# Kernel tuning notes

Hardware: AMD Instinct MI355X
Metric: run time of the kernel (lower is better)

The kernel has to match this reference:

```python
import jax, jax.numpy as jnp
import numpy as np

B, N, D = 4, 2048, 1024
H, HD = 16, 64
MAX_SEQ = 4096
INNER = H * HD


def setup_inputs() -> dict:
    key = jax.random.key(0)
    ks = jax.random.split(key, 5)
    s = 0.02
    return {
        "x": jax.random.normal(ks[0], (B, N, D), dtype=jnp.float32),
        "ln_gamma": jnp.ones((D,), jnp.float32),
        "ln_beta": jnp.zeros((D,), jnp.float32),
        "w_qkv": jax.random.normal(ks[1], (D, 3 * INNER), dtype=jnp.float32) * s,
        "w_out": jax.random.normal(ks[2], (INNER, D), dtype=jnp.float32) * s,
        "b_out": jnp.zeros((D,), jnp.float32),
    }


def _rope_tables(n, head_dim):
    inv_freq = 1.0 / (10000.0 ** (jnp.arange(0, head_dim, 2, dtype=jnp.float32) / head_dim))
    pos = jnp.arange(n, dtype=jnp.float32)
    ang = pos[:, None] * inv_freq[None, :]  # [n, hd/2]
    return jnp.sin(ang), jnp.cos(ang)


def reference(x, ln_gamma, ln_beta, w_qkv, w_out, b_out):
    b, n, d = x.shape
    # LayerNorm
    mu = jnp.mean(x, axis=-1, keepdims=True)
    var = jnp.var(x, axis=-1, keepdims=True)
    xn = (x - mu) / jnp.sqrt(var + 1e-5) * ln_gamma + ln_beta
    # QKV projection (no bias)
    qkv = xn @ w_qkv  # [b, n, 3*inner]
    q, k, v = jnp.split(qkv, 3, axis=-1)
    def to_heads(t):
        return t.reshape(b, n, H, HD).transpose(0, 2, 1, 3)  # b h n d
    q, k, v = to_heads(q), to_heads(k), to_heads(v)
    # RoPE (half-split rotation, as in source)
    sin, cos = _rope_tables(n, HD)  # [n, hd/2]
    sin = sin[None, None]
    cos = cos[None, None]
    half = HD // 2
    def rotate(t):
        t1, t2 = t[..., :half], t[..., half:]
        return jnp.concatenate([t1 * cos - t2 * sin, t2 * cos + t1 * sin], axis=-1)
    qr, kr = rotate(q), rotate(k)
    scale = HD ** -0.5
    scores = jnp.einsum('bhid,bhjd->bhij', qr, kr) * scale
    probs = jax.nn.softmax(scores, axis=-1)
    out = jnp.einsum('bhij,bhjd->bhid', probs, v)
    out = out.transpose(0, 2, 1, 3).reshape(b, n, INNER)
    return out @ w_out + b_out
```

## Files before the change

kernel.cpp:

```cpp
#include <hip/hip_runtime.h>
#include <hip/hip_bf16.h>

#define Bb   4
#define Nn   2048
#define Dd   1024
#define Hh   16
#define HDd  64
#define IN3  3072
#define RR   8192

typedef __attribute__((ext_vector_type(8))) short short8;
typedef __attribute__((ext_vector_type(4))) float floatx4;

#define MFMA16(a, b, c) __builtin_amdgcn_mfma_f32_16x16x32_bf16((a), (b), (c), 0, 0, 0)

static __device__ __forceinline__ unsigned short f2bf(float f) {
    union { float f; unsigned int u; } v; v.f = f;
    unsigned int r = v.u + 0x7fffu + ((v.u >> 16) & 1u);
    return (unsigned short)(r >> 16);
}
static __device__ __forceinline__ float bf2f(unsigned short h) {
    union { unsigned int u; float f; } v; v.u = ((unsigned int)h) << 16;
    return v.f;
}

static __device__ __forceinline__ float fast_exp2(float x) {
#if __has_builtin(__builtin_amdgcn_exp2f)
    return __builtin_amdgcn_exp2f(x);
#else
    return exp2f(x);
#endif
}

static __device__ __forceinline__ void sincos_rev(float ang, float& s, float& c) {
#if __has_builtin(__builtin_amdgcn_sinf) && __has_builtin(__builtin_amdgcn_cosf)
    float rev = ang * 0.15915494309189535f;
    rev = rev - floorf(rev);
    s = __builtin_amdgcn_sinf(rev);
    c = __builtin_amdgcn_cosf(rev);
#else
    s = sinf(ang);
    c = cosf(ang);
#endif
}

typedef const __attribute__((address_space(1))) void* gas1_t;
typedef __attribute__((address_space(3))) void* las3_t;
static __device__ __forceinline__ void load_lds16(const void* g, void* l) {
    __builtin_amdgcn_global_load_lds((gas1_t)(unsigned long long)g,
                                     (las3_t)(unsigned int)(unsigned long long)l,
                                     16, 0, 0);
}

__global__ void transpose_w(const float* __restrict__ src, unsigned short* __restrict__ dst,
                            int rows, int cols) {
    __shared__ float tile[32][33];
    int c0 = blockIdx.x * 32, r0 = blockIdx.y * 32;
    int tx = threadIdx.x, ty = threadIdx.y;
#pragma unroll
    for (int i = 0; i < 4; ++i) tile[ty + 8 * i][tx] = src[(r0 + ty + 8 * i) * cols + c0 + tx];
    __syncthreads();
#pragma unroll
    for (int i = 0; i < 4; ++i) dst[(c0 + ty + 8 * i) * rows + r0 + tx] = f2bf(tile[tx][ty + 8 * i]);
}

__global__ __launch_bounds__(256) void ln_kernel(const float* __restrict__ x,
                                                 const float* __restrict__ g,
                                                 const float* __restrict__ be,
                                                 unsigned short* __restrict__ xn) {
    int row = blockIdx.x, t = threadIdx.x;
    float4 v = ((const float4*)(x + row * Dd))[t];
    float s  = v.x + v.y + v.z + v.w;
    float sq = v.x * v.x + v.y * v.y + v.z * v.z + v.w * v.w;
#pragma unroll
    for (int off = 1; off < 64; off <<= 1) { s += __shfl_xor(s, off); sq += __shfl_xor(sq, off); }
    __shared__ float ps[4], pq2[4];
    int wv = t >> 6;
    if ((t & 63) == 0) { ps[wv] = s; pq2[wv] = sq; }
    __syncthreads();
    s  = ps[0] + ps[1] + ps[2] + ps[3];
    sq = pq2[0] + pq2[1] + pq2[2] + pq2[3];
    float mu   = s * (1.0f / Dd);
    float var  = sq * (1.0f / Dd) - mu * mu;
    float rstd = rsqrtf(var + 1e-5f);
    float4 gg = ((const float4*)g)[t];
    float4 bb = ((const float4*)be)[t];
    ushort4 o;
    o.x = f2bf((v.x - mu) * rstd * gg.x + bb.x);
    o.y = f2bf((v.y - mu) * rstd * gg.y + bb.y);
    o.z = f2bf((v.z - mu) * rstd * gg.z + bb.z);
    o.w = f2bf((v.w - mu) * rstd * gg.w + bb.w);
    ((ushort4*)(xn + row * Dd))[t] = o;
}

__global__ __launch_bounds__(512, 2) void gemm_qkv(const unsigned short* __restrict__ A,
                                                   const unsigned short* __restrict__ Bt,
                                                   unsigned short* __restrict__ qo,
                                                   unsigned short* __restrict__ ko,
                                                   unsigned short* __restrict__ vo) {
    __shared__ unsigned short LDS[65536];
    int r0 = blockIdx.x * 256, c0 = blockIdx.y * 256;
    int tid = threadIdx.x;
    int wv = tid >> 6, lane = tid & 63, l15 = lane & 15, quad = lane >> 4;
    int wm = wv >> 2, wn = wv & 3;

    floatx4 acc[8][4] = {};
    int swz0 = (quad ^ (l15 & 7)) << 3;
    int swz1 = ((4 | quad) ^ (l15 & 7)) << 3;
    const int abase = wm * 8192 + l15 * 64;
    const int bbase = 16384 + (wn >> 1) * 8192 + ((wn & 1) * 64 + l15) * 64;

    auto stageA = [&](int tt, int half) {
        unsigned short* base = &LDS[(tt & 1) * 32768 + half * 8192];
        int k0 = tt * 64;
#pragma unroll
        for (int i = 0; i < 2; ++i) {
            int q = (wv * 2 + i) * 64 + lane;
            int row = q >> 3, cp = q & 7;
            int sc = cp ^ (row & 7);
            load_lds16(&A[(r0 + half * 128 + row) * 1024 + k0 + sc * 8], &base[q * 8]);
        }
    };
    auto stageB = [&](int tt, int half) {
        unsigned short* base = &LDS[(tt & 1) * 32768 + 16384 + half * 8192];
        int k0 = tt * 64;
#pragma unroll
        for (int i = 0; i < 2; ++i) {
            int q = (wv * 2 + i) * 64 + lane;
            int row = q >> 3, cp = q & 7;
            int sc = cp ^ (row & 7);
            load_lds16(&Bt[(c0 + half * 128 + row) * 1024 + k0 + sc * 8], &base[q * 8]);
        }
    };

    stageA(0, 0); stageA(0, 1); stageB(0, 0); stageB(0, 1);
    stageA(1, 0); stageA(1, 1);
    asm volatile("s_waitcnt vmcnt(4)" ::: "memory");
    __builtin_amdgcn_s_barrier();

    for (int t = 0; t < 16; ++t) {
        int bufo = (t & 1) * 32768;
        short8 a0[4][2], a1[4][2], b0[2][2], b1[2][2];

        if (t < 15) stageB(t + 1, 0);
#pragma unroll
        for (int mi = 0; mi < 4; ++mi) {
            a0[mi][0] = *(const short8*)&LDS[bufo + abase + (mi * 16) * 64 + swz0];
            a0[mi][1] = *(const short8*)&LDS[bufo + abase + (mi * 16) * 64 + swz1];
        }
#pragma unroll
        for (int ni = 0; ni < 2; ++ni) {
            b0[ni][0] = *(const short8*)&LDS[bufo + bbase + (ni * 16) * 64 + swz0];
            b0[ni][1] = *(const short8*)&LDS[bufo + bbase + (ni * 16) * 64 + swz1];
        }
        __builtin_amdgcn_s_barrier();
        asm volatile("s_waitcnt lgkmcnt(0)" ::: "memory");
        __builtin_amdgcn_s_setprio(1);
#pragma unroll
        for (int ks = 0; ks < 2; ++ks)
#pragma unroll
            for (int mi = 0; mi < 4; ++mi)
#pragma unroll
                for (int ni = 0; ni < 2; ++ni)
                    acc[mi][ni] = MFMA16(a0[mi][ks], b0[ni][ks], acc[mi][ni]);
        __builtin_amdgcn_s_setprio(0);
        __builtin_amdgcn_s_barrier();

        if (t < 15) stageB(t + 1, 1);
#pragma unroll
        for (int mi = 0; mi < 4; ++mi) {
            a1[mi][0] = *(const short8*)&LDS[bufo + abase + ((64 + mi * 16)) * 64 + swz0];
            a1[mi][1] = *(const short8*)&LDS[bufo + abase + ((64 + mi * 16)) * 64 + swz1];
        }
        __builtin_amdgcn_s_barrier();
        asm volatile("s_waitcnt lgkmcnt(0)" ::: "memory");
        __builtin_amdgcn_s_setprio(1);
#pragma unroll
        for (int ks = 0; ks < 2; ++ks)
#pragma unroll
            for (int mi = 0; mi < 4; ++mi)
#pragma unroll
                for (int ni = 0; ni < 2; ++ni)
                    acc[4 + mi][ni] = MFMA16(a1[mi][ks], b0[ni][ks], acc[4 + mi][ni]);
        __builtin_amdgcn_s_setprio(0);
        __builtin_amdgcn_s_barrier();

        if (t < 14) stageA(t + 2, 0);
#pragma unroll
        for (int ni = 0; ni < 2; ++ni) {
            b1[ni][0] = *(const short8*)&LDS[bufo + bbase + ((32 + ni * 16)) * 64 + swz0];
            b1[ni][1] = *(const short8*)&LDS[bufo + bbase + ((32 + ni * 16)) * 64 + swz1];
        }
        __builtin_amdgcn_s_barrier();
        asm volatile("s_waitcnt lgkmcnt(0)" ::: "memory");
        __builtin_amdgcn_s_setprio(1);
#pragma unroll
        for (int ks = 0; ks < 2; ++ks)
#pragma unroll
            for (int mi = 0; mi < 4; ++mi)
#pragma unroll
                for (int ni = 0; ni < 2; ++ni)
                    acc[4 + mi][2 + ni] = MFMA16(a1[mi][ks], b1[ni][ks], acc[4 + mi][2 + ni]);
        __builtin_amdgcn_s_setprio(0);
        __builtin_amdgcn_s_barrier();

        if (t < 14) stageA(t + 2, 1);
        __builtin_amdgcn_s_barrier();
        asm volatile("s_waitcnt lgkmcnt(0)" ::: "memory");
        __builtin_amdgcn_s_setprio(1);
#pragma unroll
        for (int ks = 0; ks < 2; ++ks)
#pragma unroll
            for (int mi = 0; mi < 4; ++mi)
#pragma unroll
                for (int ni = 0; ni < 2; ++ni)
                    acc[mi][2 + ni] = MFMA16(a0[mi][ks], b1[ni][ks], acc[mi][2 + ni]);
        __builtin_amdgcn_s_setprio(0);
        if (t < 14)       asm volatile("s_waitcnt vmcnt(4)" ::: "memory");
        else if (t == 14) asm volatile("s_waitcnt vmcnt(0)" ::: "memory");
        __builtin_amdgcn_s_barrier();
    }

    if (c0 < 2048) {
        const float crope = 13.287712379549449f / 32.0f;
        float invf0 = fast_exp2(-(float)l15 * crope);
        float invf1 = fast_exp2(-(float)(l15 + 16) * crope);
#pragma unroll
        for (int mi = 0; mi < 8; ++mi)
#pragma unroll
            for (int r2 = 0; r2 < 4; ++r2) {
                int rr = r0 + wm * 128 + mi * 16 + quad * 4 + r2;
                float n = (float)(rr & 2047);
                float s0, c0r, s1, c1r;
                sincos_rev(n * invf0, s0, c0r);
                sincos_rev(n * invf1, s1, c1r);
                float t1a = acc[mi][0][r2], t2a = acc[mi][2][r2];
                acc[mi][0][r2] = t1a * c0r - t2a * s0;
                acc[mi][2][r2] = t2a * c0r + t1a * s0;
                float t1b = acc[mi][1][r2], t2b = acc[mi][3][r2];
                acc[mi][1][r2] = t1b * c1r - t2b * s1;
                acc[mi][3][r2] = t2b * c1r + t1b * s1;
            }
    }
    if (c0 < 1024) {
        const float qsc = 0.125f * 1.4426950408889634f;
#pragma unroll
        for (int mi = 0; mi < 8; ++mi)
#pragma unroll
            for (int ni = 0; ni < 4; ++ni)
#pragma unroll
                for (int r2 = 0; r2 < 4; ++r2) acc[mi][ni][r2] *= qsc;
    }
    unsigned short* outp = (c0 < 1024) ? qo : (c0 < 2048) ? ko : vo;
#pragma unroll
    for (int ni = 0; ni < 4; ++ni) {
        int c = c0 + wn * 64 + ni * 16 + l15;
        int cin = c & 1023;
        int h = cin >> 6, j = cin & 63;
#pragma unroll
        for (int mi = 0; mi < 8; ++mi) {
#pragma unroll
            for (int r2 = 0; r2 < 4; ++r2) {
                int rr = r0 + wm * 128 + mi * 16 + quad * 4 + r2;
                int b = rr >> 11, n = rr & 2047;
                int bh = b * 16 + h;
                outp[(bh * 2048 + n) * 64 + j] = f2bf(acc[mi][ni][r2]);
            }
        }
    }
}

__global__ __launch_bounds__(256) void vtrans(const unsigned short* __restrict__ v,
                                              unsigned short* __restrict__ vt) {
    __shared__ unsigned short T[64][72];
    int bh = blockIdx.y, n0 = blockIdx.x * 64;
    int t = threadIdx.x;
    int nl = t >> 2, c = (t & 3) * 16;
    const unsigned short* src = v + ((bh * 2048) + n0 + nl) * 64 + c;
    *(short8*)&T[nl][c]     = *(const short8*)src;
    *(short8*)&T[nl][c + 8] = *(const short8*)(src + 8);
    __syncthreads();
    int hd = t >> 2, nc = (t & 3) * 16;
    unsigned short tmp[16];
#pragma unroll
    for (int i = 0; i < 16; ++i) {
        int pos = nc + i;
        int blk = pos >> 5, p = pos & 31;
        int kq = (p >> 3) & 3, hh = (p >> 2) & 1, r = p & 3;
        tmp[i] = T[blk * 32 + hh * 16 + kq * 4 + r][hd];
    }
    unsigned short* dst = vt + ((bh * 64) + hd) * 2048 + n0 + nc;
    *(short8*)dst       = *(const short8*)&tmp[0];
    *(short8*)(dst + 8) = *(const short8*)&tmp[8];
}

__global__ __launch_bounds__(256, 3) void attn_kernel(const unsigned short* __restrict__ q,
                                                      const unsigned short* __restrict__ k,
                                                      const unsigned short* __restrict__ vt,
                                                      unsigned short* __restrict__ attn) {
    __shared__ unsigned short KVs[2][2][64 * 64];
    int fid = blockIdx.x;
    int xcd = fid & 7, rest = fid >> 3;
    int qi = rest & 15, bhg = rest >> 4;
    int bh = bhg * 8 + xcd;
    int q0 = qi * 128;
    int tid = threadIdx.x;
    int wave = tid >> 6, lane = tid & 63, l15 = lane & 15, quad = lane >> 4;
    const unsigned short* qb  = q  + bh * (Nn * HDd);
    const unsigned short* kbp = k  + bh * (Nn * HDd);
    const unsigned short* vb  = vt + bh * (HDd * Nn);
    int qbase = q0 + wave * 32;

    short8 bq[2][2];
#pragma unroll
    for (int g = 0; g < 2; ++g) {
        bq[g][0] = *(const short8*)&qb[(qbase + g * 16 + l15) * 64 + quad * 8];
        bq[g][1] = *(const short8*)&qb[(qbase + g * 16 + l15) * 64 + 32 + quad * 8];
    }

    auto stage = [&](int buf, int kb0) {
#pragma unroll
        for (int i = 0; i < 2; ++i) {
            int c = wave * 2 + i;
            int p = c * 64 + lane;
            int row = p >> 3, pr = p & 7;
            int sc = pr ^ (row & 7);
            load_lds16(&kbp[(kb0 + row) * 64 + sc * 8], &KVs[buf][0][p * 8]);
            load_lds16(&vb[row * Nn + kb0 + sc * 8],    &KVs[buf][1][p * 8]);
        }
    };

    floatx4 ot[2][4] = {};
    float l_run[2] = {0.0f, 0.0f};
    int swz0 = (quad ^ (l15 & 7)) << 3;
    int swz1 = ((4 | quad) ^ (l15 & 7)) << 3;

    auto body = [&](int cur, int kt) {
        if (kt < 31) stage(cur ^ 1, (kt + 1) * 64);
        const unsigned short* Kc = KVs[cur][0];
        const unsigned short* Vc = KVs[cur][1];
        short8 ka0[4], ka1[4];
#pragma unroll
        for (int mb = 0; mb < 4; ++mb) {
            ka0[mb] = *(const short8*)&Kc[(mb * 16 + l15) * 64 + swz0];
            ka1[mb] = *(const short8*)&Kc[(mb * 16 + l15) * 64 + swz1];
        }
        short8 bv0[4], bv1[4];
#pragma unroll
        for (int ht = 0; ht < 4; ++ht) {
            int row = (ht * 16 + l15) * 64;
            bv0[ht] = *(const short8*)&Vc[row + swz0];
            bv1[ht] = *(const short8*)&Vc[row + swz1];
        }
#pragma unroll
        for (int g = 0; g < 2; ++g) {
            floatx4 st[4];
#pragma unroll
            for (int mb = 0; mb < 4; ++mb) {
                floatx4 z = {0.0f, 0.0f, 0.0f, 0.0f};
                z = MFMA16(ka0[mb], bq[g][0], z);
                st[mb] = MFMA16(ka1[mb], bq[g][1], z);
            }
            short8 pa[2];
            float sump = 0.0f;
#pragma unroll
            for (int c = 0; c < 2; ++c) {
                union { ushort4 u[2]; short8 s; } w;
#pragma unroll
                for (int t2 = 0; t2 < 2; ++t2) {
                    int mb = 2 * c + t2;
                    float p0 = fast_exp2(st[mb][0]);
                    float p1 = fast_exp2(st[mb][1]);
                    float p2 = fast_exp2(st[mb][2]);
                    float p3 = fast_exp2(st[mb][3]);
                    sump += (p0 + p1) + (p2 + p3);
                    *(__hip_bfloat162*)&w.u[t2].x = __float22bfloat162_rn(float2{p0, p1});
                    *(__hip_bfloat162*)&w.u[t2].z = __float22bfloat162_rn(float2{p2, p3});
                }
                pa[c] = w.s;
            }
            l_run[g] += sump;
#pragma unroll
            for (int ht = 0; ht < 4; ++ht) {
                ot[g][ht] = MFMA16(pa[0], bv0[ht], ot[g][ht]);
                ot[g][ht] = MFMA16(pa[1], bv1[ht], ot[g][ht]);
            }
        }
        __syncthreads();
    };

    stage(0, 0);
    __syncthreads();
    for (int kt = 0; kt < 32; kt += 2) {
        body(0, kt);
        body(1, kt + 1);
    }
    int b = bh >> 4, h = bh & 15;
    unsigned short* ob = ((unsigned short*)KVs) + wave * 1152;
#pragma unroll
    for (int g = 0; g < 2; ++g) {
        float l = l_run[g];
        l += __shfl_xor(l, 16);
        l += __shfl_xor(l, 32);
        float invl = 1.0f / l;
        float il[4];
#pragma unroll
        for (int r = 0; r < 4; ++r) il[r] = __shfl(invl, quad * 4 + r);
#pragma unroll
        for (int ht = 0; ht < 4; ++ht)
#pragma unroll
            for (int r = 0; r < 4; ++r)
                ob[(quad * 4 + r) * 72 + ht * 16 + l15] = f2bf(ot[g][ht][r] * il[r]);
        int q_loc = lane >> 2, seg = lane & 3;
        unsigned short* dst = attn + ((long)(b * Nn + q0 + wave * 32 + g * 16 + q_loc)) * 1024 + h * 64 + seg * 16;
        *(short8*)dst       = *(const short8*)&ob[q_loc * 72 + seg * 16];
        *(short8*)(dst + 8) = *(const short8*)&ob[q_loc * 72 + seg * 16 + 8];
    }
}

__global__ __launch_bounds__(256) void gemm_out(const unsigned short* __restrict__ A,
                                                const unsigned short* __restrict__ Bt,
                                                const float* __restrict__ bout,
                                                float* __restrict__ out) {
    __shared__ unsigned short As[128 * 64];
    __shared__ unsigned short Bs[128 * 64];
    int r0 = blockIdx.x * 128, c0 = blockIdx.y * 128;
    int tid = threadIdx.x;
    int wave = tid >> 6, lane = tid & 63, l15 = lane & 15, quad = lane >> 4;
    int wm = wave & 1, wn = wave >> 1;
    floatx4 acc[4][4] = {};
    int swz0 = (quad ^ (l15 & 7)) << 3;
    int swz1 = ((4 | quad) ^ (l15 & 7)) << 3;
    for (int k0 = 0; k0 < 1024; k0 += 64) {
#pragma unroll
        for (int i = 0; i < 4; ++i) {
            int c = wave * 4 + i;
            int p = c * 64 + lane;
            int row = p >> 3, pr = p & 7;
            int sc = pr ^ (row & 7);
            load_lds16(&A[(r0 + row) * 1024 + k0 + sc * 8],  &As[p * 8]);
            load_lds16(&Bt[(c0 + row) * 1024 + k0 + sc * 8], &Bs[p * 8]);
        }
        __syncthreads();
#pragma unroll
        for (int ks = 0; ks < 2; ++ks) {
            int sw = ks ? swz1 : swz0;
            short8 af[4], bf[4];
#pragma unroll
            for (int mi = 0; mi < 4; ++mi)
                af[mi] = *(const short8*)&As[(wm * 64 + mi * 16 + l15) * 64 + sw];
#pragma unroll
            for (int ni = 0; ni < 4; ++ni)
                bf[ni] = *(const short8*)&Bs[(wn * 64 + ni * 16 + l15) * 64 + sw];
#pragma unroll
            for (int mi = 0; mi < 4; ++mi)
#pragma unroll
                for (int ni = 0; ni < 4; ++ni)
                    acc[mi][ni] = MFMA16(af[mi], bf[ni], acc[mi][ni]);
        }
        __syncthreads();
    }
#pragma unroll
    for (int ni = 0; ni < 4; ++ni) {
        int c = c0 + wn * 64 + ni * 16 + l15;
        float bias = bout[c];
#pragma unroll
        for (int mi = 0; mi < 4; ++mi)
#pragma unroll
            for (int r2 = 0; r2 < 4; ++r2) {
                int rr = r0 + wm * 64 + mi * 16 + quad * 4 + r2;
                out[rr * 1024 + c] = acc[mi][ni][r2] + bias;
            }
    }
}

extern "C" void kernel_launch(void* const* d_in, const int* in_sizes, int n_in,
                              void* d_out, int out_size, void* d_ws, size_t ws_size,
                              hipStream_t stream) {
    const float* x    = (const float*)d_in[0];
    const float* g    = (const float*)d_in[1];
    const float* be   = (const float*)d_in[2];
    const float* wqkv = (const float*)d_in[3];
    const float* wout = (const float*)d_in[4];
    const float* bout = (const float*)d_in[5];
    float* out = (float*)d_out;

    char* ws = (char*)d_ws;
    unsigned short* xn    = (unsigned short*)(ws);
    unsigned short* wqkvT = (unsigned short*)(ws + 16777216);
    unsigned short* woutT = (unsigned short*)(ws + 23068672);
    unsigned short* qb    = (unsigned short*)(ws + 25165824);
    unsigned short* kb    = (unsigned short*)(ws + 41943040);
    unsigned short* vt    = (unsigned short*)(ws + 58720256);
    unsigned short* attn  = (unsigned short*)(ws + 75497472);
    unsigned short* vtmp  = attn;

    transpose_w<<<dim3(IN3 / 32, Dd / 32), dim3(32, 8), 0, stream>>>(wqkv, wqkvT, Dd, IN3);
    transpose_w<<<dim3(Dd / 32, Dd / 32), dim3(32, 8), 0, stream>>>(wout, woutT, Dd, Dd);
    ln_kernel<<<RR, 256, 0, stream>>>(x, g, be, xn);
    gemm_qkv<<<dim3(RR / 256, IN3 / 256), 512, 0, stream>>>(xn, wqkvT, qb, kb, vtmp);
    vtrans<<<dim3(Nn / 64, Bb * Hh), 256, 0, stream>>>(vtmp, vt);
    attn_kernel<<<dim3(Nn / 128 * Bb * Hh), 256, 0, stream>>>(qb, kb, vt, attn);
    gemm_out<<<dim3(RR / 128, Dd / 128), 256, 0, stream>>>(attn, woutT, bout, out);
}
```

Baseline: 266.1 us.

## Triple-buffer K/V staging with vmcnt waits and MFMA row-sum

Moves the attention kernel's K/V LDS staging from double to triple buffering, prefetching two tiles ahead and replacing __syncthreads with targeted s_waitcnt vmcnt plus s_barrier, so global loads overlap more compute. The softmax denominator is now accumulated on the matrix cores by multiplying P against a ones vector, instead of scalar adds followed by cross-lane shuffles. s_setprio hints are placed around the MFMA sections. LDS use grows by half, which may reduce occupancy at the 3-blocks-per-CU launch bound, and the row sum is taken from bf16-rounded probabilities.

```diff
diff --git a/kernel.cpp b/kernel.cpp
--- a/kernel.cpp
+++ b/kernel.cpp
@@ -298,7 +298,7 @@
                                                       const unsigned short* __restrict__ k,
                                                       const unsigned short* __restrict__ vt,
                                                       unsigned short* __restrict__ attn) {
-    __shared__ unsigned short KVs[2][2][64 * 64];
+    __shared__ unsigned short KVs[3][2][64 * 64];
     int fid = blockIdx.x;
     int xcd = fid & 7, rest = fid >> 3;
     int qi = rest & 15, bhg = rest >> 4;
@@ -331,12 +331,15 @@
     };
 
     floatx4 ot[2][4] = {};
-    float l_run[2] = {0.0f, 0.0f};
+    floatx4 osum[2] = {};
+    const floatx4 fz = {0.0f, 0.0f, 0.0f, 0.0f};
+    const short8 vones = {(short)0x3F80, (short)0x3F80, (short)0x3F80, (short)0x3F80,
+                          (short)0x3F80, (short)0x3F80, (short)0x3F80, (short)0x3F80};
     int swz0 = (quad ^ (l15 & 7)) << 3;
     int swz1 = ((4 | quad) ^ (l15 & 7)) << 3;
 
-    auto body = [&](int cur, int kt) {
-        if (kt < 31) stage(cur ^ 1, (kt + 1) * 64);
+    auto body = [&](int cur, int nxt, int kt) {
+        if (kt + 2 < 32) stage(nxt, (kt + 2) * 64);
         const unsigned short* Kc = KVs[cur][0];
         const unsigned short* Vc = KVs[cur][1];
         short8 ka0[4], ka1[4];
@@ -355,14 +358,14 @@
 #pragma unroll
         for (int g = 0; g < 2; ++g) {
             floatx4 st[4];
+            __builtin_amdgcn_s_setprio(1);
 #pragma unroll
             for (int mb = 0; mb < 4; ++mb) {
-                floatx4 z = {0.0f, 0.0f, 0.0f, 0.0f};
-                z = MFMA16(ka0[mb], bq[g][0], z);
+                floatx4 z = MFMA16(ka0[mb], bq[g][0], fz);
                 st[mb] = MFMA16(ka1[mb], bq[g][1], z);
             }
+            __builtin_amdgcn_s_setprio(0);
             short8 pa[2];
-            float sump = 0.0f;
 #pragma unroll
             for (int c = 0; c < 2; ++c) {
                 union { ushort4 u[2]; short8 s; } w;
@@ -373,39 +376,45 @@
                     float p1 = fast_exp2(st[mb][1]);
                     float p2 = fast_exp2(st[mb][2]);
                     float p3 = fast_exp2(st[mb][3]);
-                    sump += (p0 + p1) + (p2 + p3);
                     *(__hip_bfloat162*)&w.u[t2].x = __float22bfloat162_rn(float2{p0, p1});
                     *(__hip_bfloat162*)&w.u[t2].z = __float22bfloat162_rn(float2{p2, p3});
                 }
                 pa[c] = w.s;
             }
-            l_run[g] += sump;
+            __builtin_amdgcn_s_setprio(1);
+            osum[g] = MFMA16(pa[0], vones, osum[g]);
+            osum[g] = MFMA16(pa[1], vones, osum[g]);
 #pragma unroll
             for (int ht = 0; ht < 4; ++ht) {
                 ot[g][ht] = MFMA16(pa[0], bv0[ht], ot[g][ht]);
                 ot[g][ht] = MFMA16(pa[1], bv1[ht], ot[g][ht]);
             }
-        }
-        __syncthreads();
+            __builtin_amdgcn_s_setprio(0);
+        }
+        if (kt < 30)       asm volatile("s_waitcnt vmcnt(4)" ::: "memory");
+        else if (kt == 30) asm volatile("s_waitcnt vmcnt(0)" ::: "memory");
+        __builtin_amdgcn_s_barrier();
     };
 
     stage(0, 0);
-    __syncthreads();
-    for (int kt = 0; kt < 32; kt += 2) {
-        body(0, kt);
-        body(1, kt + 1);
-    }
+    stage(1, 64);
+    asm volatile("s_waitcnt vmcnt(4)" ::: "memory");
+    __builtin_amdgcn_s_barrier();
+    for (int kt = 0; kt < 30; kt += 3) {
+        body(0, 2, kt);
+        body(1, 0, kt + 1);
+        body(2, 1, kt + 2);
+    }
+    body(0, 2, 30);
+    body(1, 0, 31);
+
     int b = bh >> 4, h = bh & 15;
     unsigned short* ob = ((unsigned short*)KVs) + wave * 1152;
 #pragma unroll
     for (int g = 0; g < 2; ++g) {
-        float l = l_run[g];
-        l += __shfl_xor(l, 16);
-        l += __shfl_xor(l, 32);
-        float invl = 1.0f / l;
         float il[4];
 #pragma unroll
-        for (int r = 0; r < 4; ++r) il[r] = __shfl(invl, quad * 4 + r);
+        for (int r = 0; r < 4; ++r) il[r] = 1.0f / osum[g][r];
 #pragma unroll
         for (int ht = 0; ht < 4; ++ht)
 #pragma unroll
```

New measurement: 272.8 us. +2.5%, slower.
